# Optimization experiments

Hardware: AMD Instinct MI355X
Metric: run time of the kernel (lower is better)

## Reference

```python
import jax, jax.numpy as jnp
import numpy as np

B, N, DIM = 16, 1024, 512
H, DH = 8, 64  # heads, dim_head; inner_dim = H*DH = 512
MASK_VAL = -1e-9  # value ASSIGNED (not added) to diagonal, per original code


def setup_inputs() -> dict:
    key = jax.random.key(0)
    ks = jax.random.split(key, 8)
    w = 0.02  # small init so softmax is not saturated
    x = jax.random.normal(ks[0], (B, N, DIM), dtype=jnp.float32)
    Wq = jax.random.normal(ks[1], (DIM, H * DH), dtype=jnp.float32) * w
    Wkv = jax.random.normal(ks[2], (DIM, 2 * H * DH), dtype=jnp.float32) * w
    scale = jnp.full((H,), DH ** -0.5, dtype=jnp.float32)  # nn.Parameter(scale*ones(heads))
    mix_pre = jax.random.normal(ks[3], (H, H), dtype=jnp.float32) * w
    mix_post = jax.random.normal(ks[4], (H, H), dtype=jnp.float32) * w
    Wout = jax.random.normal(ks[5], (H * DH, DIM), dtype=jnp.float32) * w
    bout = jnp.zeros((DIM,), dtype=jnp.float32)
    return {"x": x, "Wq": Wq, "Wkv": Wkv, "scale": scale,
            "mix_pre": mix_pre, "mix_post": mix_post, "Wout": Wout, "bout": bout}


def reference(x, Wq, Wkv, scale, mix_pre, mix_post, Wout, bout):
    b, n, _ = x.shape
    # projections -> [b, h, n, d]
    q = (x @ Wq).reshape(b, n, H, DH).transpose(0, 2, 1, 3)
    kv = (x @ Wkv).reshape(b, n, 2, H, DH)
    k = kv[:, :, 0].transpose(0, 2, 1, 3)
    v = kv[:, :, 1].transpose(0, 2, 1, 3)
    # LMSA: per-head learned scale
    dots = jnp.einsum('bhid,bhjd->bhij', q, k) * scale[None, :, None, None]
    # if_patch_attn: set diagonal entries to -1e-9 (assignment, as in torch)
    eye = jnp.eye(n, dtype=bool)
    dots = jnp.where(eye, jnp.float32(MASK_VAL), dots)
    # talking heads: pre-softmax head mix
    dots = jnp.einsum('bhij,hg->bgij', dots, mix_pre)
    attn = jax.nn.softmax(dots, axis=-1)
    # post-softmax head mix
    attn = jnp.einsum('bhij,hg->bgij', attn, mix_post)
    out = jnp.einsum('bhij,bhjd->bhid', attn, v)  # [b,h,n,d]
    out = out.transpose(0, 2, 1, 3).reshape(b, n, H * DH)
    return out @ Wout + bout
```

## Files before the change

### kernel.cpp

```cpp
#include <hip/hip_runtime.h>
#include <math.h>


typedef short bf16x8 __attribute__((ext_vector_type(8)));
typedef float f32x4 __attribute__((ext_vector_type(4)));

__device__ __forceinline__ f32x4 mfma16(bf16x8 a, bf16x8 b, f32x4 c) {
  return __builtin_amdgcn_mfma_f32_16x16x32_bf16(a, b, c, 0, 0, 0);
}

__device__ __forceinline__ unsigned short f2bf(float f) {
  unsigned u = __float_as_uint(f);
  u = (u + 0x7fffu + ((u >> 16) & 1u)) >> 16;
  return (unsigned short)u;
}

__device__ __forceinline__ void splitbf(float f, unsigned short& hi,
                                        unsigned short& lo) {
  hi = f2bf(f);
  float fh = __uint_as_float((unsigned)hi << 16);
  lo = f2bf(f - fh);
}

__device__ __forceinline__ f32x4 zero4() {
  f32x4 z = {0.f, 0.f, 0.f, 0.f};
  return z;
}

namespace {

constexpr int kB = 16, kN = 1024, kH = 8;

__global__ __launch_bounds__(256) void prep(
    const float* __restrict__ Wq, const float* __restrict__ Wkv,
    const float* __restrict__ Wout, unsigned short* __restrict__ WTh,
    unsigned short* __restrict__ WTl, unsigned short* __restrict__ WoTh,
    unsigned short* __restrict__ WoTl) {
  int id = blockIdx.x * 256 + threadIdx.x;
  unsigned short h, l;
  if (id < 1536 * 512) {
    int n = id >> 9, k = id & 511;
    float v = (n < 512) ? Wq[(size_t)k * 512 + n]
                        : Wkv[(size_t)k * 1024 + (n - 512)];
    splitbf(v, h, l);
    WTh[id] = h; WTl[id] = l;
  } else {
    int id2 = id - 1536 * 512;
    int n = id2 >> 9, k = id2 & 511;
    splitbf(Wout[(size_t)k * 512 + n], h, l);
    WoTh[id2] = h; WoTl[id2] = l;
  }
}

__global__ __launch_bounds__(256) void gemm_qkv(
    const float* __restrict__ X, const unsigned short* __restrict__ WTh,
    const unsigned short* __restrict__ WTl, const float* __restrict__ scale,
    unsigned short* __restrict__ Qh, unsigned short* __restrict__ Ql,
    unsigned short* __restrict__ Kh, unsigned short* __restrict__ Kl,
    unsigned short* __restrict__ Vh, unsigned short* __restrict__ Vl) {
  __shared__ unsigned short Ah[128 * 72], Al[128 * 72];
  __shared__ unsigned short Bh[128 * 72], Bl[128 * 72];
  const int tid = threadIdx.x;
  const int n0 = blockIdx.x * 128, m0 = blockIdx.y * 128;
  const int w = tid >> 6, lane = tid & 63, quad = lane >> 4, ln = lane & 15;
  const int mw = (w >> 1) * 64, nw = (w & 1) * 64;
  const int srow = tid >> 3, schk = (tid & 7) * 8;
  f32x4 acc[4][4];
#pragma unroll
  for (int i = 0; i < 4; ++i)
#pragma unroll
    for (int j = 0; j < 4; ++j) acc[i][j] = zero4();
  for (int k0 = 0; k0 < 512; k0 += 64) {
    float xa[4][8];
    uint4 bh4[4], bl4[4];
#pragma unroll
    for (int c2 = 0; c2 < 4; ++c2) {
      const float* xs = X + (size_t)(m0 + c2 * 32 + srow) * 512 + k0 + schk;
      *(float4*)&xa[c2][0] = *(const float4*)xs;
      *(float4*)&xa[c2][4] = *(const float4*)(xs + 4);
      size_t boff = (size_t)(n0 + c2 * 32 + srow) * 512 + k0 + schk;
      bh4[c2] = *(const uint4*)(WTh + boff);
      bl4[c2] = *(const uint4*)(WTl + boff);
    }
    __syncthreads();
#pragma unroll
    for (int c2 = 0; c2 < 4; ++c2) {
      unsigned short hh[8], ll[8];
#pragma unroll
      for (int e = 0; e < 8; ++e) splitbf(xa[c2][e], hh[e], ll[e]);
      uint4 ph, pl;
      ph.x = hh[0] | ((unsigned)hh[1] << 16); pl.x = ll[0] | ((unsigned)ll[1] << 16);
      ph.y = hh[2] | ((unsigned)hh[3] << 16); pl.y = ll[2] | ((unsigned)ll[3] << 16);
      ph.z = hh[4] | ((unsigned)hh[5] << 16); pl.z = ll[4] | ((unsigned)ll[5] << 16);
      ph.w = hh[6] | ((unsigned)hh[7] << 16); pl.w = ll[6] | ((unsigned)ll[7] << 16);
      *(uint4*)&Ah[(c2 * 32 + srow) * 72 + schk] = ph;
      *(uint4*)&Al[(c2 * 32 + srow) * 72 + schk] = pl;
      *(uint4*)&Bh[(c2 * 32 + srow) * 72 + schk] = bh4[c2];
      *(uint4*)&Bl[(c2 * 32 + srow) * 72 + schk] = bl4[c2];
    }
    __syncthreads();
#pragma unroll
    for (int ks = 0; ks < 2; ++ks) {
      bf16x8 afh[4], afl[4], bfh[4], bfl[4];
#pragma unroll
      for (int t = 0; t < 4; ++t) {
        int ao = (mw + t * 16 + ln) * 72 + ks * 32 + quad * 8;
        int bo = (nw + t * 16 + ln) * 72 + ks * 32 + quad * 8;
        afh[t] = *(const bf16x8*)&Ah[ao];
        afl[t] = *(const bf16x8*)&Al[ao];
        bfh[t] = *(const bf16x8*)&Bh[bo];
        bfl[t] = *(const bf16x8*)&Bl[bo];
      }
#pragma unroll
      for (int mt = 0; mt < 4; ++mt)
#pragma unroll
        for (int nt = 0; nt < 4; ++nt) {
          acc[mt][nt] = mfma16(afh[mt], bfh[nt], acc[mt][nt]);
          acc[mt][nt] = mfma16(afh[mt], bfl[nt], acc[mt][nt]);
          acc[mt][nt] = mfma16(afl[mt], bfh[nt], acc[mt][nt]);
        }
    }
  }
  const int region = n0 >> 9;
#pragma unroll
  for (int nt = 0; nt < 4; ++nt) {
    const int col = n0 + nw + nt * 16 + ln;
    const int local = col - region * 512;
    const int hh = local >> 6, d = local & 63;
    const float sc = (region == 0) ? scale[hh] : 1.f;
#pragma unroll
    for (int mt = 0; mt < 4; ++mt) {
#pragma unroll
      for (int r = 0; r < 4; ++r) {
        const int row = m0 + mw + mt * 16 + quad * 4 + r;
        const int b = row >> 10, i = row & 1023;
        unsigned short vh, vl;
        splitbf(acc[mt][nt][r] * sc, vh, vl);
        if (region == 0) {
          size_t o = (((size_t)(b * 8 + hh) * 1024 + i) << 6) + d;
          Qh[o] = vh; Ql[o] = vl;
        } else if (region == 1) {
          size_t o = (((size_t)(b * 8 + hh) * 1024 + i) << 6) + d;
          Kh[o] = vh; Kl[o] = vl;
        } else {
          size_t o = (((size_t)(b * 8 + hh) * 64 + d) << 10) + i;
          Vh[o] = vh; Vl[o] = vl;
        }
      }
    }
  }
}

__global__ __launch_bounds__(128) void attn_fused(
    const unsigned short* __restrict__ Qh_g, const unsigned short* __restrict__ Ql_g,
    const unsigned short* __restrict__ Kh, const unsigned short* __restrict__ Kl,
    const unsigned short* __restrict__ Vh, const unsigned short* __restrict__ Vl,
    const float* __restrict__ mix_pre, const float* __restrict__ mix_post,
    float* __restrict__ OA) {
  __shared__ unsigned short Qsh[128 * 72];
  __shared__ unsigned short Wsh[128 * 40], Wsl[128 * 40];
  __shared__ float mixp_s[64], mixq_s[64], dfix_s[8];
  __shared__ float Ils[8][16];
  float* lred = (float*)Wsh;
  const int tid = threadIdx.x;
  const int b = blockIdx.y, i0 = blockIdx.x * 16;
  const int w = tid >> 6, lane = tid & 63, quad = lane >> 4, ln = lane & 15;
  const int jh = w * 16;
  if (tid < 64) { mixp_s[tid] = mix_pre[tid]; mixq_s[tid] = mix_post[tid]; }
  if (tid < 8) {
    float s = 0.f;
#pragma unroll
    for (int h = 0; h < 8; ++h) s += mix_pre[h * 8 + tid];
    dfix_s[tid] = -1e-9f * s;
  }
#pragma unroll
  for (int c = 0; c < 8; ++c) {
    int v = tid + 128 * c;
    int row = v >> 3, chk = (v & 7) * 8;
    int h = row >> 4, ii = row & 15;
    *(uint4*)&Qsh[row * 72 + chk] =
        *(const uint4*)(Qh_g + (((size_t)(b * 8 + h) * 1024 + i0 + ii) << 6) + chk);
  }
  bf16x8 qlo[8][2];
#pragma unroll
  for (int h = 0; h < 8; ++h)
#pragma unroll
    for (int ks = 0; ks < 2; ++ks)
      qlo[h][ks] = *(const bf16x8*)(
          Ql_g + (((size_t)(b * 8 + h) * 1024 + i0 + ln) << 6) + ks * 32 + quad * 8);
  __syncthreads();
  const int ig0 = i0 + quad * 4;

  float l[8][4];
#pragma unroll
  for (int a = 0; a < 8; ++a)
#pragma unroll
    for (int r = 0; r < 4; ++r) l[a][r] = 0.f;
  for (int j0 = 0; j0 < 1024; j0 += 32) {
    bf16x8 kh_r[2][2], kl_r[2][2];
#pragma unroll
    for (int ks = 0; ks < 2; ++ks) {
      size_t kro = (((size_t)(b * 8 + 0) * 1024 + j0 + jh + ln) << 6) + ks * 32 + quad * 8;
      kh_r[0][ks] = *(const bf16x8*)(Kh + kro);
      kl_r[0][ks] = *(const bf16x8*)(Kl + kro);
    }
    f32x4 S[8];
    int cur = 0;
#pragma unroll
    for (int h = 0; h < 8; ++h) {
      const int nxt = cur ^ 1;
      if (h < 7) {
#pragma unroll
        for (int ks = 0; ks < 2; ++ks) {
          size_t kro = (((size_t)(b * 8 + h + 1) * 1024 + j0 + jh + ln) << 6) + ks * 32 + quad * 8;
          kh_r[nxt][ks] = *(const bf16x8*)(Kh + kro);
          kl_r[nxt][ks] = *(const bf16x8*)(Kl + kro);
        }
      }
      f32x4 acc = zero4();
#pragma unroll
      for (int ks = 0; ks < 2; ++ks) {
        bf16x8 ah = *(const bf16x8*)&Qsh[(h * 16 + ln) * 72 + ks * 32 + quad * 8];
        acc = mfma16(ah, kh_r[cur][ks], acc);
        acc = mfma16(ah, kl_r[cur][ks], acc);
        acc = mfma16(qlo[h][ks], kh_r[cur][ks], acc);
      }
      S[h] = acc;
      cur = nxt;
    }
    const int dr = (j0 + jh + ln) - ig0;
#pragma unroll
    for (int a = 0; a < 8; ++a) {
      f32x4 sm = S[0] * mixp_s[a];
#pragma unroll
      for (int h = 1; h < 8; ++h) sm += S[h] * mixp_s[h * 8 + a];
      const float df = dfix_s[a];
#pragma unroll
      for (int r = 0; r < 4; ++r) {
        float v = (r == dr) ? df : sm[r];
        l[a][r] += __expf(v);
      }
    }
  }
#pragma unroll
  for (int off = 1; off < 16; off <<= 1)
#pragma unroll
    for (int a = 0; a < 8; ++a)
#pragma unroll
      for (int r = 0; r < 4; ++r) l[a][r] += __shfl_xor(l[a][r], off);
  if (ln == 0) {
#pragma unroll
    for (int a = 0; a < 8; ++a)
#pragma unroll
      for (int r = 0; r < 4; ++r) lred[(w * 8 + a) * 16 + quad * 4 + r] = l[a][r];
  }
  __syncthreads();
  {
    int a = tid >> 4, i = tid & 15;
    Ils[a][i] = 1.f / (lred[a * 16 + i] + lred[(8 + a) * 16 + i]);
  }
  __syncthreads();

  f32x4 O[4][4];
#pragma unroll
  for (int cc = 0; cc < 4; ++cc)
#pragma unroll
    for (int nt = 0; nt < 4; ++nt) O[cc][nt] = zero4();
  for (int j0 = 0; j0 < 1024; j0 += 32) {
    bf16x8 kh_r[2][2], kl_r[2][2];
#pragma unroll
    for (int ks = 0; ks < 2; ++ks) {
      size_t kro = (((size_t)(b * 8 + 0) * 1024 + j0 + jh + ln) << 6) + ks * 32 + quad * 8;
      kh_r[0][ks] = *(const bf16x8*)(Kh + kro);
      kl_r[0][ks] = *(const bf16x8*)(Kl + kro);
    }
    f32x4 S[8];
    int cur = 0;
#pragma unroll
    for (int h = 0; h < 8; ++h) {
      const int nxt = cur ^ 1;
      if (h < 7) {
#pragma unroll
        for (int ks = 0; ks < 2; ++ks) {
          size_t kro = (((size_t)(b * 8 + h + 1) * 1024 + j0 + jh + ln) << 6) + ks * 32 + quad * 8;
          kh_r[nxt][ks] = *(const bf16x8*)(Kh + kro);
          kl_r[nxt][ks] = *(const bf16x8*)(Kl + kro);
        }
      }
      f32x4 acc = zero4();
#pragma unroll
      for (int ks = 0; ks < 2; ++ks) {
        bf16x8 ah = *(const bf16x8*)&Qsh[(h * 16 + ln) * 72 + ks * 32 + quad * 8];
        acc = mfma16(ah, kh_r[cur][ks], acc);
        acc = mfma16(ah, kl_r[cur][ks], acc);
        acc = mfma16(qlo[h][ks], kh_r[cur][ks], acc);
      }
      S[h] = acc;
      cur = nxt;
    }
    const int dr = (j0 + jh + ln) - ig0;
    f32x4 P[8];
#pragma unroll
    for (int a = 0; a < 8; ++a) {
      f32x4 sm = S[0] * mixp_s[a];
#pragma unroll
      for (int h = 1; h < 8; ++h) sm += S[h] * mixp_s[h * 8 + a];
      const float df = dfix_s[a];
      f32x4 il4 = *(const f32x4*)&Ils[a][quad * 4];
      f32x4 p;
#pragma unroll
      for (int r = 0; r < 4; ++r) {
        float v = (r == dr) ? df : sm[r];
        p[r] = __expf(v) * il4[r];
      }
      P[a] = p;
    }
#pragma unroll
    for (int c = 0; c < 8; ++c) {
      f32x4 wv = P[0] * mixq_s[c];
#pragma unroll
      for (int a = 1; a < 8; ++a) wv += P[a] * mixq_s[a * 8 + c];
#pragma unroll
      for (int r = 0; r < 4; ++r) {
        unsigned short vh, vl;
        splitbf(wv[r], vh, vl);
        int o = (c * 16 + quad * 4 + r) * 40 + jh + ln;
        Wsh[o] = vh; Wsl[o] = vl;
      }
    }
    bf16x8 vbh[2][4], vbl[2][4];
    {
      const int c = w * 4;
#pragma unroll
      for (int nt = 0; nt < 4; ++nt) {
        size_t vo = (((size_t)(b * 8 + c) * 64 + nt * 16 + ln) << 10) + j0 + quad * 8;
        vbh[0][nt] = *(const bf16x8*)(Vh + vo);
        vbl[0][nt] = *(const bf16x8*)(Vl + vo);
      }
    }
    __syncthreads();
    int vcur = 0;
#pragma unroll
    for (int cc = 0; cc < 4; ++cc) {
      const int c = w * 4 + cc;
      const int vnxt = vcur ^ 1;
      if (cc < 3) {
#pragma unroll
        for (int nt = 0; nt < 4; ++nt) {
          size_t vo = (((size_t)(b * 8 + c + 1) * 64 + nt * 16 + ln) << 10) + j0 + quad * 8;
          vbh[vnxt][nt] = *(const bf16x8*)(Vh + vo);
          vbl[vnxt][nt] = *(const bf16x8*)(Vl + vo);
        }
      }
      bf16x8 a_h = *(const bf16x8*)&Wsh[(c * 16 + ln) * 40 + quad * 8];
      bf16x8 a_l = *(const bf16x8*)&Wsl[(c * 16 + ln) * 40 + quad * 8];
#pragma unroll
      for (int nt = 0; nt < 4; ++nt) {
        O[cc][nt] = mfma16(a_h, vbh[vcur][nt], O[cc][nt]);
        O[cc][nt] = mfma16(a_h, vbl[vcur][nt], O[cc][nt]);
        O[cc][nt] = mfma16(a_l, vbh[vcur][nt], O[cc][nt]);
      }
      vcur = vnxt;
    }
    __syncthreads();
  }
#pragma unroll
  for (int cc = 0; cc < 4; ++cc)
#pragma unroll
    for (int nt = 0; nt < 4; ++nt)
#pragma unroll
      for (int r = 0; r < 4; ++r) {
        const int i = i0 + quad * 4 + r;
        const int col = (w * 4 + cc) * 64 + nt * 16 + ln;
        OA[((size_t)(b * 1024 + i) << 9) + col] = O[cc][nt][r];
      }
}

__global__ __launch_bounds__(256) void gemm_out(
    const float* __restrict__ A, const unsigned short* __restrict__ BTh,
    const unsigned short* __restrict__ BTl, const float* __restrict__ bias,
    float* __restrict__ Out) {
  __shared__ unsigned short Ah[128 * 72], Al[128 * 72];
  __shared__ unsigned short Bh[128 * 72], Bl[128 * 72];
  const int tid = threadIdx.x;
  const int n0 = blockIdx.x * 128, m0 = blockIdx.y * 128;
  const int w = tid >> 6, lane = tid & 63, quad = lane >> 4, ln = lane & 15;
  const int mw = (w >> 1) * 64, nw = (w & 1) * 64;
  const int srow = tid >> 3, schk = (tid & 7) * 8;
  f32x4 acc[4][4];
#pragma unroll
  for (int i = 0; i < 4; ++i)
#pragma unroll
    for (int j = 0; j < 4; ++j) acc[i][j] = zero4();
  for (int k0 = 0; k0 < 512; k0 += 64) {
    float xa[4][8];
    uint4 bh4[4], bl4[4];
#pragma unroll
    for (int c2 = 0; c2 < 4; ++c2) {
      const float* xs = A + (size_t)(m0 + c2 * 32 + srow) * 512 + k0 + schk;
      *(float4*)&xa[c2][0] = *(const float4*)xs;
      *(float4*)&xa[c2][4] = *(const float4*)(xs + 4);
      size_t boff = (size_t)(n0 + c2 * 32 + srow) * 512 + k0 + schk;
      bh4[c2] = *(const uint4*)(BTh + boff);
      bl4[c2] = *(const uint4*)(BTl + boff);
    }
    __syncthreads();
#pragma unroll
    for (int c2 = 0; c2 < 4; ++c2) {
      unsigned short hh[8], ll[8];
#pragma unroll
      for (int e = 0; e < 8; ++e) splitbf(xa[c2][e], hh[e], ll[e]);
      uint4 ph, pl;
      ph.x = hh[0] | ((unsigned)hh[1] << 16); pl.x = ll[0] | ((unsigned)ll[1] << 16);
      ph.y = hh[2] | ((unsigned)hh[3] << 16); pl.y = ll[2] | ((unsigned)ll[3] << 16);
      ph.z = hh[4] | ((unsigned)hh[5] << 16); pl.z = ll[4] | ((unsigned)ll[5] << 16);
      ph.w = hh[6] | ((unsigned)hh[7] << 16); pl.w = ll[6] | ((unsigned)ll[7] << 16);
      *(uint4*)&Ah[(c2 * 32 + srow) * 72 + schk] = ph;
      *(uint4*)&Al[(c2 * 32 + srow) * 72 + schk] = pl;
      *(uint4*)&Bh[(c2 * 32 + srow) * 72 + schk] = bh4[c2];
      *(uint4*)&Bl[(c2 * 32 + srow) * 72 + schk] = bl4[c2];
    }
    __syncthreads();
#pragma unroll
    for (int ks = 0; ks < 2; ++ks) {
      bf16x8 afh[4], afl[4], bfh[4], bfl[4];
#pragma unroll
      for (int t = 0; t < 4; ++t) {
        int ao = (mw + t * 16 + ln) * 72 + ks * 32 + quad * 8;
        int bo = (nw + t * 16 + ln) * 72 + ks * 32 + quad * 8;
        afh[t] = *(const bf16x8*)&Ah[ao];
        afl[t] = *(const bf16x8*)&Al[ao];
        bfh[t] = *(const bf16x8*)&Bh[bo];
        bfl[t] = *(const bf16x8*)&Bl[bo];
      }
#pragma unroll
      for (int mt = 0; mt < 4; ++mt)
#pragma unroll
        for (int nt = 0; nt < 4; ++nt) {
          acc[mt][nt] = mfma16(afh[mt], bfh[nt], acc[mt][nt]);
          acc[mt][nt] = mfma16(afh[mt], bfl[nt], acc[mt][nt]);
          acc[mt][nt] = mfma16(afl[mt], bfh[nt], acc[mt][nt]);
        }
    }
  }
#pragma unroll
  for (int nt = 0; nt < 4; ++nt) {
    const int col = n0 + nw + nt * 16 + ln;
    const float bcol = bias[col];
#pragma unroll
    for (int mt = 0; mt < 4; ++mt) {
#pragma unroll
      for (int r = 0; r < 4; ++r) {
        const int row = m0 + mw + mt * 16 + quad * 4 + r;
        Out[(size_t)row * 512 + col] = acc[mt][nt][r] + bcol;
      }
    }
  }
}

}

extern "C" void kernel_launch(void* const* d_in, const int* in_sizes, int n_in,
                              void* d_out, int out_size, void* d_ws, size_t ws_size,
                              hipStream_t stream) {
  const float* x        = (const float*)d_in[0];
  const float* Wq       = (const float*)d_in[1];
  const float* Wkv      = (const float*)d_in[2];
  const float* scale    = (const float*)d_in[3];
  const float* mix_pre  = (const float*)d_in[4];
  const float* mix_post = (const float*)d_in[5];
  const float* Wout     = (const float*)d_in[6];
  const float* bout     = (const float*)d_in[7];
  float* out = (float*)d_out;

  char* p = (char*)d_ws;
  const size_t qsz = (size_t)kB * kH * kN * 64;
  unsigned short* WTh  = (unsigned short*)p; p += (size_t)1536 * 512 * 2;
  unsigned short* WTl  = (unsigned short*)p; p += (size_t)1536 * 512 * 2;
  unsigned short* WoTh = (unsigned short*)p; p += (size_t)512 * 512 * 2;
  unsigned short* WoTl = (unsigned short*)p; p += (size_t)512 * 512 * 2;
  unsigned short* Qh   = (unsigned short*)p; p += qsz * 2;
  unsigned short* Ql   = (unsigned short*)p; p += qsz * 2;
  unsigned short* Kh   = (unsigned short*)p; p += qsz * 2;
  unsigned short* Kl   = (unsigned short*)p; p += qsz * 2;
  unsigned short* Vh   = (unsigned short*)p; p += qsz * 2;
  unsigned short* Vl   = (unsigned short*)p; p += qsz * 2;
  float* OA = (float*)p; p += (size_t)kB * kN * 512 * 4;

  prep<<<4096, 256, 0, stream>>>(Wq, Wkv, Wout, WTh, WTl, WoTh, WoTl);
  gemm_qkv<<<dim3(12, 128), 256, 0, stream>>>(x, WTh, WTl, scale,
                                              Qh, Ql, Kh, Kl, Vh, Vl);
  attn_fused<<<dim3(64, 16), 128, 0, stream>>>(Qh, Ql, Kh, Kl, Vh, Vl,
                                               mix_pre, mix_post, OA);
  gemm_out<<<dim3(4, 128), 256, 0, stream>>>(OA, WoTh, WoTl, bout, out);
}
```

Measured before the change: 1.435 ms.

## Drop split-bf16 for Q/K, enlarge attention tile to 32 rows with 256 threads

Q and K are now stored as a single bf16 instead of hi/lo pairs, so QK^T drops from three MFMAs per k-step to one. Q fragments stay in registers instead of going through shared memory. The attention block grows to 32 query rows over 4 waves (2 row groups by 2 key halves), and the pre-softmax head mix is accumulated per head as scores are produced. The grid order becomes batch-major, and the post-mix weights are split by truncation rather than rounding. The main risk is accuracy: the logits lose precision that the split-bf16 scheme used to keep.

Result: slower. 1.679 ms (+17.0%).

```diff
diff --git a/kernel.cpp b/kernel.cpp
--- a/kernel.cpp
+++ b/kernel.cpp
@@ -20,6 +20,14 @@
   hi = f2bf(f);
   float fh = __uint_as_float((unsigned)hi << 16);
   lo = f2bf(f - fh);
+}
+
+__device__ __forceinline__ void splitbf_t(float f, unsigned short& hi,
+                                          unsigned short& lo) {
+  unsigned u = __float_as_uint(f);
+  hi = (unsigned short)(u >> 16);
+  float fh = __uint_as_float(u & 0xFFFF0000u);
+  lo = (unsigned short)(__float_as_uint(f - fh) >> 16);
 }
 
 __device__ __forceinline__ f32x4 zero4() {
@@ -55,8 +63,7 @@
 __global__ __launch_bounds__(256) void gemm_qkv(
     const float* __restrict__ X, const unsigned short* __restrict__ WTh,
     const unsigned short* __restrict__ WTl, const float* __restrict__ scale,
-    unsigned short* __restrict__ Qh, unsigned short* __restrict__ Ql,
-    unsigned short* __restrict__ Kh, unsigned short* __restrict__ Kl,
+    unsigned short* __restrict__ Qb, unsigned short* __restrict__ Kb,
     unsigned short* __restrict__ Vh, unsigned short* __restrict__ Vl) {
   __shared__ unsigned short Ah[128 * 72], Al[128 * 72];
   __shared__ unsigned short Bh[128 * 72], Bl[128 * 72];
@@ -134,15 +141,14 @@
       for (int r = 0; r < 4; ++r) {
         const int row = m0 + mw + mt * 16 + quad * 4 + r;
         const int b = row >> 10, i = row & 1023;
-        unsigned short vh, vl;
-        splitbf(acc[mt][nt][r] * sc, vh, vl);
+        const float v = acc[mt][nt][r];
         if (region == 0) {
-          size_t o = (((size_t)(b * 8 + hh) * 1024 + i) << 6) + d;
-          Qh[o] = vh; Ql[o] = vl;
+          Qb[(((size_t)(b * 8 + hh) * 1024 + i) << 6) + d] = f2bf(v * sc);
         } else if (region == 1) {
-          size_t o = (((size_t)(b * 8 + hh) * 1024 + i) << 6) + d;
-          Kh[o] = vh; Kl[o] = vl;
+          Kb[(((size_t)(b * 8 + hh) * 1024 + i) << 6) + d] = f2bf(v);
         } else {
+          unsigned short vh, vl;
+          splitbf(v, vh, vl);
           size_t o = (((size_t)(b * 8 + hh) * 64 + d) << 10) + i;
           Vh[o] = vh; Vl[o] = vl;
         }
@@ -151,45 +157,41 @@
   }
 }
 
-__global__ __launch_bounds__(128) void attn_fused(
-    const unsigned short* __restrict__ Qh_g, const unsigned short* __restrict__ Ql_g,
-    const unsigned short* __restrict__ Kh, const unsigned short* __restrict__ Kl,
+__global__ __launch_bounds__(256, 2) void attn_fused(
+    const unsigned short* __restrict__ Qb, const unsigned short* __restrict__ Kb,
     const unsigned short* __restrict__ Vh, const unsigned short* __restrict__ Vl,
     const float* __restrict__ mix_pre, const float* __restrict__ mix_post,
     float* __restrict__ OA) {
-  __shared__ unsigned short Qsh[128 * 72];
-  __shared__ unsigned short Wsh[128 * 40], Wsl[128 * 40];
-  __shared__ float mixp_s[64], mixq_s[64], dfix_s[8];
-  __shared__ float Ils[8][16];
+  __shared__ unsigned short Wsh[256 * 40], Wsl[256 * 40];
+  __shared__ float mixp_s[64];
+  __shared__ float mixqT_s[64];
+  __shared__ float dfix_s[8];
+  __shared__ float Ils[8][32];
   float* lred = (float*)Wsh;
   const int tid = threadIdx.x;
-  const int b = blockIdx.y, i0 = blockIdx.x * 16;
+  const int b = blockIdx.x, i0 = blockIdx.y * 32;
   const int w = tid >> 6, lane = tid & 63, quad = lane >> 4, ln = lane & 15;
-  const int jh = w * 16;
-  if (tid < 64) { mixp_s[tid] = mix_pre[tid]; mixq_s[tid] = mix_post[tid]; }
+  const int ih = w >> 1, jh = w & 1;
+  const int irow0 = ih * 16;
+  if (tid < 64) {
+    mixp_s[tid] = mix_pre[tid];
+    mixqT_s[tid] = mix_post[(tid & 7) * 8 + (tid >> 3)];
+  }
   if (tid < 8) {
     float s = 0.f;
 #pragma unroll
     for (int h = 0; h < 8; ++h) s += mix_pre[h * 8 + tid];
     dfix_s[tid] = -1e-9f * s;
   }
-#pragma unroll
-  for (int c = 0; c < 8; ++c) {
-    int v = tid + 128 * c;
-    int row = v >> 3, chk = (v & 7) * 8;
-    int h = row >> 4, ii = row & 15;
-    *(uint4*)&Qsh[row * 72 + chk] =
-        *(const uint4*)(Qh_g + (((size_t)(b * 8 + h) * 1024 + i0 + ii) << 6) + chk);
-  }
-  bf16x8 qlo[8][2];
+  bf16x8 qf[8][2];
 #pragma unroll
   for (int h = 0; h < 8; ++h)
 #pragma unroll
     for (int ks = 0; ks < 2; ++ks)
-      qlo[h][ks] = *(const bf16x8*)(
-          Ql_g + (((size_t)(b * 8 + h) * 1024 + i0 + ln) << 6) + ks * 32 + quad * 8);
+      qf[h][ks] = *(const bf16x8*)(
+          Qb + (((size_t)(b * 8 + h) * 1024 + i0 + irow0 + ln) << 6) + ks * 32 + quad * 8);
   __syncthreads();
-  const int ig0 = i0 + quad * 4;
+  const int ibase = i0 + irow0 + quad * 4;
 
   float l[8][4];
 #pragma unroll
@@ -197,47 +199,35 @@
 #pragma unroll
     for (int r = 0; r < 4; ++r) l[a][r] = 0.f;
   for (int j0 = 0; j0 < 1024; j0 += 32) {
-    bf16x8 kh_r[2][2], kl_r[2][2];
-#pragma unroll
-    for (int ks = 0; ks < 2; ++ks) {
-      size_t kro = (((size_t)(b * 8 + 0) * 1024 + j0 + jh + ln) << 6) + ks * 32 + quad * 8;
-      kh_r[0][ks] = *(const bf16x8*)(Kh + kro);
-      kl_r[0][ks] = *(const bf16x8*)(Kl + kro);
-    }
-    f32x4 S[8];
-    int cur = 0;
+    bf16x8 kf[8][2];
+#pragma unroll
+    for (int h = 0; h < 8; ++h)
+#pragma unroll
+      for (int ks = 0; ks < 2; ++ks)
+        kf[h][ks] = *(const bf16x8*)(
+            Kb + (((size_t)(b * 8 + h) * 1024 + j0 + jh * 16 + ln) << 6) + ks * 32 + quad * 8);
+    f32x4 smix[8];
+#pragma unroll
+    for (int a = 0; a < 8; ++a) smix[a] = zero4();
 #pragma unroll
     for (int h = 0; h < 8; ++h) {
-      const int nxt = cur ^ 1;
-      if (h < 7) {
-#pragma unroll
-        for (int ks = 0; ks < 2; ++ks) {
-          size_t kro = (((size_t)(b * 8 + h + 1) * 1024 + j0 + jh + ln) << 6) + ks * 32 + quad * 8;
-          kh_r[nxt][ks] = *(const bf16x8*)(Kh + kro);
-          kl_r[nxt][ks] = *(const bf16x8*)(Kl + kro);
-        }
-      }
-      f32x4 acc = zero4();
-#pragma unroll
-      for (int ks = 0; ks < 2; ++ks) {
-        bf16x8 ah = *(const bf16x8*)&Qsh[(h * 16 + ln) * 72 + ks * 32 + quad * 8];
-        acc = mfma16(ah, kh_r[cur][ks], acc);
-        acc = mfma16(ah, kl_r[cur][ks], acc);
-        acc = mfma16(qlo[h][ks], kh_r[cur][ks], acc);
-      }
-      S[h] = acc;
-      cur = nxt;
-    }
-    const int dr = (j0 + jh + ln) - ig0;
+      f32x4 Sh = mfma16(qf[h][0], kf[h][0], zero4());
+      Sh = mfma16(qf[h][1], kf[h][1], Sh);
+      f32x4 mp0 = *(const f32x4*)&mixp_s[h * 8];
+      f32x4 mp1 = *(const f32x4*)&mixp_s[h * 8 + 4];
+#pragma unroll
+      for (int a = 0; a < 4; ++a) {
+        smix[a] += Sh * mp0[a];
+        smix[4 + a] += Sh * mp1[a];
+      }
+    }
+    const int dr = (j0 + jh * 16 + ln) - ibase;
 #pragma unroll
     for (int a = 0; a < 8; ++a) {
-      f32x4 sm = S[0] * mixp_s[a];
-#pragma unroll
-      for (int h = 1; h < 8; ++h) sm += S[h] * mixp_s[h * 8 + a];
       const float df = dfix_s[a];
 #pragma unroll
       for (int r = 0; r < 4; ++r) {
-        float v = (r == dr) ? df : sm[r];
+        float v = (r == dr) ? df : smix[a][r];
         l[a][r] += __expf(v);
       }
     }
@@ -252,12 +242,13 @@
 #pragma unroll
     for (int a = 0; a < 8; ++a)
 #pragma unroll
-      for (int r = 0; r < 4; ++r) lred[(w * 8 + a) * 16 + quad * 4 + r] = l[a][r];
+      for (int r = 0; r < 4; ++r)
+        lred[(jh * 8 + a) * 32 + irow0 + quad * 4 + r] = l[a][r];
   }
   __syncthreads();
   {
-    int a = tid >> 4, i = tid & 15;
-    Ils[a][i] = 1.f / (lred[a * 16 + i] + lred[(8 + a) * 16 + i]);
+    const int a = tid >> 5, i = tid & 31;
+    Ils[a][i] = 1.f / (lred[a * 32 + i] + lred[(8 + a) * 32 + i]);
   }
   __syncthreads();
 
@@ -267,82 +258,91 @@
 #pragma unroll
     for (int nt = 0; nt < 4; ++nt) O[cc][nt] = zero4();
   for (int j0 = 0; j0 < 1024; j0 += 32) {
-    bf16x8 kh_r[2][2], kl_r[2][2];
-#pragma unroll
-    for (int ks = 0; ks < 2; ++ks) {
-      size_t kro = (((size_t)(b * 8 + 0) * 1024 + j0 + jh + ln) << 6) + ks * 32 + quad * 8;
-      kh_r[0][ks] = *(const bf16x8*)(Kh + kro);
-      kl_r[0][ks] = *(const bf16x8*)(Kl + kro);
-    }
-    f32x4 S[8];
-    int cur = 0;
-#pragma unroll
-    for (int h = 0; h < 8; ++h) {
-      const int nxt = cur ^ 1;
-      if (h < 7) {
-#pragma unroll
-        for (int ks = 0; ks < 2; ++ks) {
-          size_t kro = (((size_t)(b * 8 + h + 1) * 1024 + j0 + jh + ln) << 6) + ks * 32 + quad * 8;
-          kh_r[nxt][ks] = *(const bf16x8*)(Kh + kro);
-          kl_r[nxt][ks] = *(const bf16x8*)(Kl + kro);
-        }
-      }
-      f32x4 acc = zero4();
-#pragma unroll
-      for (int ks = 0; ks < 2; ++ks) {
-        bf16x8 ah = *(const bf16x8*)&Qsh[(h * 16 + ln) * 72 + ks * 32 + quad * 8];
-        acc = mfma16(ah, kh_r[cur][ks], acc);
-        acc = mfma16(ah, kl_r[cur][ks], acc);
-        acc = mfma16(qlo[h][ks], kh_r[cur][ks], acc);
-      }
-      S[h] = acc;
-      cur = nxt;
-    }
-    const int dr = (j0 + jh + ln) - ig0;
+    f32x4 smix[8];
+#pragma unroll
+    for (int a = 0; a < 8; ++a) smix[a] = zero4();
+    bf16x8 kf[4][2];
+#pragma unroll
+    for (int hh = 0; hh < 4; ++hh)
+#pragma unroll
+      for (int ks = 0; ks < 2; ++ks)
+        kf[hh][ks] = *(const bf16x8*)(
+            Kb + (((size_t)(b * 8 + hh) * 1024 + j0 + jh * 16 + ln) << 6) + ks * 32 + quad * 8);
+#pragma unroll
+    for (int hh = 0; hh < 4; ++hh) {
+      f32x4 Sh = mfma16(qf[hh][0], kf[hh][0], zero4());
+      Sh = mfma16(qf[hh][1], kf[hh][1], Sh);
+      f32x4 mp0 = *(const f32x4*)&mixp_s[hh * 8];
+      f32x4 mp1 = *(const f32x4*)&mixp_s[hh * 8 + 4];
+#pragma unroll
+      for (int a = 0; a < 4; ++a) {
+        smix[a] += Sh * mp0[a];
+        smix[4 + a] += Sh * mp1[a];
+      }
+    }
+#pragma unroll
+    for (int hh = 0; hh < 4; ++hh)
+#pragma unroll
+      for (int ks = 0; ks < 2; ++ks)
+        kf[hh][ks] = *(const bf16x8*)(
+            Kb + (((size_t)(b * 8 + hh + 4) * 1024 + j0 + jh * 16 + ln) << 6) + ks * 32 + quad * 8);
+#pragma unroll
+    for (int hh = 0; hh < 4; ++hh) {
+      const int h = hh + 4;
+      f32x4 Sh = mfma16(qf[h][0], kf[hh][0], zero4());
+      Sh = mfma16(qf[h][1], kf[hh][1], Sh);
+      f32x4 mp0 = *(const f32x4*)&mixp_s[h * 8];
+      f32x4 mp1 = *(const f32x4*)&mixp_s[h * 8 + 4];
+#pragma unroll
+      for (int a = 0; a < 4; ++a) {
+        smix[a] += Sh * mp0[a];
+        smix[4 + a] += Sh * mp1[a];
+      }
+    }
+    const int dr = (j0 + jh * 16 + ln) - ibase;
     f32x4 P[8];
 #pragma unroll
     for (int a = 0; a < 8; ++a) {
-      f32x4 sm = S[0] * mixp_s[a];
-#pragma unroll
-      for (int h = 1; h < 8; ++h) sm += S[h] * mixp_s[h * 8 + a];
       const float df = dfix_s[a];
-      f32x4 il4 = *(const f32x4*)&Ils[a][quad * 4];
+      f32x4 il4 = *(const f32x4*)&Ils[a][irow0 + quad * 4];
       f32x4 p;
 #pragma unroll
       for (int r = 0; r < 4; ++r) {
-        float v = (r == dr) ? df : sm[r];
+        float v = (r == dr) ? df : smix[a][r];
         p[r] = __expf(v) * il4[r];
       }
       P[a] = p;
     }
 #pragma unroll
     for (int c = 0; c < 8; ++c) {
-      f32x4 wv = P[0] * mixq_s[c];
-#pragma unroll
-      for (int a = 1; a < 8; ++a) wv += P[a] * mixq_s[a * 8 + c];
-#pragma unroll
-      for (int r = 0; r < 4; ++r) {
-        unsigned short vh, vl;
-        splitbf(wv[r], vh, vl);
-        int o = (c * 16 + quad * 4 + r) * 40 + jh + ln;
-        Wsh[o] = vh; Wsl[o] = vl;
-      }
-    }
+      f32x4 mq0 = *(const f32x4*)&mixqT_s[c * 8];
+      f32x4 mq1 = *(const f32x4*)&mixqT_s[c * 8 + 4];
+      f32x4 wv = P[0] * mq0[0];
+#pragma unroll
+      for (int a = 1; a < 4; ++a) wv += P[a] * mq0[a];
+#pragma unroll
+      for (int a = 0; a < 4; ++a) wv += P[4 + a] * mq1[a];
+#pragma unroll
+      for (int r = 0; r < 4; ++r) {
+        unsigned short vh2, vl2;
+        splitbf_t(wv[r], vh2, vl2);
+        int o = (c * 32 + irow0 + quad * 4 + r) * 40 + jh * 16 + ln;
+        Wsh[o] = vh2; Wsl[o] = vl2;
+      }
+    }
+    __syncthreads();
+    const int cbase = jh * 4;
     bf16x8 vbh[2][4], vbl[2][4];
-    {
-      const int c = w * 4;
-#pragma unroll
-      for (int nt = 0; nt < 4; ++nt) {
-        size_t vo = (((size_t)(b * 8 + c) * 64 + nt * 16 + ln) << 10) + j0 + quad * 8;
-        vbh[0][nt] = *(const bf16x8*)(Vh + vo);
-        vbl[0][nt] = *(const bf16x8*)(Vl + vo);
-      }
-    }
-    __syncthreads();
+#pragma unroll
+    for (int nt = 0; nt < 4; ++nt) {
+      size_t vo = (((size_t)(b * 8 + cbase) * 64 + nt * 16 + ln) << 10) + j0 + quad * 8;
+      vbh[0][nt] = *(const bf16x8*)(Vh + vo);
+      vbl[0][nt] = *(const bf16x8*)(Vl + vo);
+    }
     int vcur = 0;
 #pragma unroll
     for (int cc = 0; cc < 4; ++cc) {
-      const int c = w * 4 + cc;
+      const int c = cbase + cc;
       const int vnxt = vcur ^ 1;
       if (cc < 3) {
 #pragma unroll
@@ -352,8 +352,8 @@
           vbl[vnxt][nt] = *(const bf16x8*)(Vl + vo);
         }
       }
-      bf16x8 a_h = *(const bf16x8*)&Wsh[(c * 16 + ln) * 40 + quad * 8];
-      bf16x8 a_l = *(const bf16x8*)&Wsl[(c * 16 + ln) * 40 + quad * 8];
+      bf16x8 a_h = *(const bf16x8*)&Wsh[(c * 32 + irow0 + ln) * 40 + quad * 8];
+      bf16x8 a_l = *(const bf16x8*)&Wsl[(c * 32 + irow0 + ln) * 40 + quad * 8];
 #pragma unroll
       for (int nt = 0; nt < 4; ++nt) {
         O[cc][nt] = mfma16(a_h, vbh[vcur][nt], O[cc][nt]);
@@ -370,8 +370,8 @@
     for (int nt = 0; nt < 4; ++nt)
 #pragma unroll
       for (int r = 0; r < 4; ++r) {
-        const int i = i0 + quad * 4 + r;
-        const int col = (w * 4 + cc) * 64 + nt * 16 + ln;
+        const int i = i0 + irow0 + quad * 4 + r;
+        const int col = (jh * 4 + cc) * 64 + nt * 16 + ln;
         OA[((size_t)(b * 1024 + i) << 9) + col] = O[cc][nt][r];
       }
 }
@@ -479,18 +479,15 @@
   unsigned short* WTl  = (unsigned short*)p; p += (size_t)1536 * 512 * 2;
   unsigned short* WoTh = (unsigned short*)p; p += (size_t)512 * 512 * 2;
   unsigned short* WoTl = (unsigned short*)p; p += (size_t)512 * 512 * 2;
-  unsigned short* Qh   = (unsigned short*)p; p += qsz * 2;
-  unsigned short* Ql   = (unsigned short*)p; p += qsz * 2;
-  unsigned short* Kh   = (unsigned short*)p; p += qsz * 2;
-  unsigned short* Kl   = (unsigned short*)p; p += qsz * 2;
+  unsigned short* Qb   = (unsigned short*)p; p += qsz * 2;
+  unsigned short* Kb   = (unsigned short*)p; p += qsz * 2;
   unsigned short* Vh   = (unsigned short*)p; p += qsz * 2;
   unsigned short* Vl   = (unsigned short*)p; p += qsz * 2;
   float* OA = (float*)p; p += (size_t)kB * kN * 512 * 4;
 
   prep<<<4096, 256, 0, stream>>>(Wq, Wkv, Wout, WTh, WTl, WoTh, WoTl);
-  gemm_qkv<<<dim3(12, 128), 256, 0, stream>>>(x, WTh, WTl, scale,
-                                              Qh, Ql, Kh, Kl, Vh, Vl);
-  attn_fused<<<dim3(64, 16), 128, 0, stream>>>(Qh, Ql, Kh, Kl, Vh, Vl,
-                                               mix_pre, mix_post, OA);
+  gemm_qkv<<<dim3(12, 128), 256, 0, stream>>>(x, WTh, WTl, scale, Qb, Kb, Vh, Vl);
+  attn_fused<<<dim3(16, 32), 256, 0, stream>>>(Qb, Kb, Vh, Vl, mix_pre,
+                                               mix_post, OA);
   gemm_out<<<dim3(4, 128), 256, 0, stream>>>(OA, WoTh, WoTl, bout, out);
 }
```
